# Performance work log

Measured on AMD Instinct MI355X. Metric: run time of the kernel, lower is better.

The kernel has to match this reference:

```python
import jax, jax.numpy as jnp
import numpy as np
import math

B, S, D, H = 4, 2048, 1024, 16
DH = D // H  # 64

def setup_inputs() -> dict:
    key = jax.random.key(0)
    ks = jax.random.split(key, 6)
    return {
        "x": jax.random.normal(ks[0], (B, S, D), dtype=jnp.float32),
        "alibi": jax.random.normal(ks[1], (1, H, S, S), dtype=jnp.float32),
        "w_qkv": jax.random.normal(ks[2], (3 * D, D), dtype=jnp.float32) * 0.02,
        "b_qkv": jax.random.normal(ks[3], (3 * D,), dtype=jnp.float32) * 0.02,
        "w_o": jax.random.normal(ks[4], (D, D), dtype=jnp.float32) * 0.02,
        "b_o": jax.random.normal(ks[5], (D,), dtype=jnp.float32) * 0.02,
    }

def reference(x, alibi, w_qkv, b_qkv, w_o, b_o):
    b, s, d = x.shape
    # torch Linear: y = x @ W.T + b
    qkv = x @ w_qkv.T + b_qkv                       # [B, S, 3D]
    qkv = qkv.reshape(b, s, H, 3, DH)               # interleaved per-head q,k,v
    q = jnp.swapaxes(qkv[:, :, :, 0, :], 1, 2)      # [B, H, S, DH]
    k = jnp.swapaxes(qkv[:, :, :, 1, :], 1, 2)
    v = jnp.swapaxes(qkv[:, :, :, 2, :], 1, 2)
    scores = jnp.einsum("bhqd,bhkd->bhqk", q, k) / math.sqrt(DH)
    attn = jax.nn.softmax(scores + alibi, axis=-1)  # [B, H, S, S]
    o = jnp.einsum("bhqk,bhkd->bhqd", attn, v)      # [B, H, S, DH]
    o = jnp.swapaxes(o, 1, 2).reshape(b, s, d)      # [B, S, D]
    return o @ w_o.T + b_o
```

## Files before the change

kernel.cpp:

```cpp
#include <hip/hip_runtime.h>
#include <stdint.h>

#define S_LEN 2048
#define NH    16
#define NB    4
#define DH    64
#define DMODEL 1024

using bf16x8 = __attribute__((ext_vector_type(8))) __bf16;
using f32x4  = __attribute__((ext_vector_type(4))) float;
using us8    = __attribute__((ext_vector_type(8))) unsigned short;

__device__ __forceinline__ unsigned short f2bf_rne(float f) {
    unsigned u = __builtin_bit_cast(unsigned, f);
    return (unsigned short)((u + 0x7FFFu + ((u >> 16) & 1u)) >> 16);
}

__device__ __forceinline__ bf16x8 ld_bf8(const unsigned short* p) {
    return __builtin_bit_cast(bf16x8, *(const us8*)p);
}

__device__ __forceinline__ f32x4 mfma16(bf16x8 a, bf16x8 b, f32x4 c) {
    return __builtin_amdgcn_mfma_f32_16x16x32_bf16(a, b, c, 0, 0, 0);
}

__device__ __forceinline__ float fast_exp2(float x) {
#if __has_builtin(__builtin_amdgcn_exp2f)
    return __builtin_amdgcn_exp2f(x);
#else
    return __expf(x * 0.69314718056f);
#endif
}

typedef __attribute__((address_space(1))) void* gp1_t;
typedef __attribute__((address_space(3))) void* lp3_t;

__device__ __forceinline__ void gload_lds16(const void* g, void* l) {
    __builtin_amdgcn_global_load_lds((gp1_t)(const_cast<void*>(g)), (lp3_t)l, 16, 0, 0);
}

#define GBAR()  asm volatile("s_barrier" ::: "memory")
#define WAIT6() asm volatile("s_waitcnt vmcnt(6)" ::: "memory")
#define WAIT0() asm volatile("s_waitcnt vmcnt(0)" ::: "memory")

__global__ void cvt_bf16(const float* __restrict__ in, unsigned short* __restrict__ out, int n4) {
    int i = blockIdx.x * 256 + threadIdx.x;
    if (i < n4) {
        float4 v = ((const float4*)in)[i];
        ushort4 o;
        o.x = f2bf_rne(v.x); o.y = f2bf_rne(v.y);
        o.z = f2bf_rne(v.z); o.w = f2bf_rne(v.w);
        ((ushort4*)out)[i] = o;
    }
}

template <int EPI>
__global__ __launch_bounds__(512, 2) void gemm256(
    const unsigned short* __restrict__ A,
    const unsigned short* __restrict__ W,
    const float* __restrict__ bias,
    float* __restrict__ outF,
    unsigned short* __restrict__ Qb,
    unsigned short* __restrict__ Kb,
    unsigned short* __restrict__ Vt,
    int nTilesN)
{
    constexpr int BM = 256, BN = 128, BK = 64;
    constexpr int MI = 4, NJ = 4;
    constexpr int AI = (BM * BK / 8) / 512;
    constexpr int BI = (BN * BK / 8) / 512;

    __shared__ __align__(16) unsigned short As[2][BM * BK];
    __shared__ __align__(16) unsigned short Bs[2][BN * BK];

    const int nwg = gridDim.x;
    const int swz = (blockIdx.x & 7) * (nwg >> 3) + (blockIdx.x >> 3);
    const int bm = swz / nTilesN;
    const int bn = swz % nTilesN;
    const int tileM = bm * BM, tileN = bn * BN;

    const int tid = threadIdx.x, lane = tid & 63, w = tid >> 6;
    const int m16 = lane & 15, quad = lane >> 4;
    const int wm = w >> 1, wn = w & 1;

    f32x4 acc[MI][NJ] = {};

    size_t aoff[AI], boff[BI];
#pragma unroll
    for (int i = 0; i < AI; i++) {
        const int u = (i * 8 + w) * 64 + lane;
        const int row = u >> 3, slot = u & 7;
        aoff[i] = (size_t)(tileM + row) * 1024 + (size_t)((slot ^ (row & 7)) * 8);
    }
#pragma unroll
    for (int i = 0; i < BI; i++) {
        const int u = (i * 8 + w) * 64 + lane;
        const int row = u >> 3, slot = u & 7;
        boff[i] = (size_t)(tileN + row) * 1024 + (size_t)((slot ^ (row & 7)) * 8);
    }

#define STAGE(buf, kk) do {                                               \
        _Pragma("unroll")                                                 \
        for (int i = 0; i < AI; i++)                                      \
            gload_lds16(A + aoff[i] + (kk), &As[buf][(i * 8 + w) * 512]); \
        _Pragma("unroll")                                                 \
        for (int i = 0; i < BI; i++)                                      \
            gload_lds16(W + boff[i] + (kk), &Bs[buf][(i * 8 + w) * 512]); \
    } while (0)

#define COMPUTE(buf) do {                                                          \
        _Pragma("unroll")                                                          \
        for (int ks = 0; ks < 2; ks++) {                                           \
            bf16x8 af[MI], bfv[NJ];                                                \
            _Pragma("unroll")                                                      \
            for (int i = 0; i < MI; i++) {                                         \
                const int R = wm * 64 + i * 16 + m16;                              \
                af[i] = ld_bf8(&As[buf][(R * 8 + ((ks * 4 + quad) ^ (R & 7))) * 8]); \
            }                                                                      \
            _Pragma("unroll")                                                      \
            for (int j = 0; j < NJ; j++) {                                         \
                const int Rb = wn * 64 + j * 16 + m16;                             \
                bfv[j] = ld_bf8(&Bs[buf][(Rb * 8 + ((ks * 4 + quad) ^ (Rb & 7))) * 8]); \
            }                                                                      \
            _Pragma("unroll")                                                      \
            for (int i = 0; i < MI; i++)                                           \
                _Pragma("unroll")                                                  \
                for (int j = 0; j < NJ; j++)                                       \
                    acc[i][j] = mfma16(af[i], bfv[j], acc[i][j]);                  \
        }                                                                          \
    } while (0)

    STAGE(0, 0);
    STAGE(1, 64);
    WAIT6();
    GBAR();

    for (int kk = 0; kk < 1024; kk += 128) {
        COMPUTE(0);
        GBAR();
        if (kk + 128 < 1024) { STAGE(0, kk + 128); WAIT6(); }
        else                 { WAIT0(); }
        GBAR();
        COMPUTE(1);
        if (kk + 128 < 1024) {
            GBAR();
            if (kk + 192 < 1024) { STAGE(1, kk + 192); WAIT6(); }
            else                 { WAIT0(); }
            GBAR();
        }
    }
#undef STAGE
#undef COMPUTE

#pragma unroll
    for (int i = 0; i < MI; i++) {
        const int mrow = tileM + wm * 64 + i * 16 + quad * 4;
#pragma unroll
        for (int j = 0; j < NJ; j++) {
            const int nb0 = tileN + wn * 64 + j * 16;
            const int n = nb0 + m16;
            const float bv = bias[n];
            if (EPI == 0) {
                const int hh = nb0 / 192, rem = nb0 % 192;
                const int t = rem / 64, dbase = rem % 64;
                const int d = dbase + m16;
#pragma unroll
                for (int r = 0; r < 4; r++) {
                    float val = acc[i][j][r] + bv;
                    const int m = mrow + r;
                    const int b_ = m >> 11, s_ = m & 2047;
                    const size_t bh = (size_t)b_ * NH + hh;
                    if (t == 0)
                        Qb[(bh * S_LEN + s_) * DH + d] = f2bf_rne(val * 0.18033688f);
                    else if (t == 1)
                        Kb[(bh * S_LEN + s_) * DH + d] = f2bf_rne(val);
                    else
                        Vt[(bh * DH + d) * S_LEN + s_] = f2bf_rne(val);
                }
            } else {
#pragma unroll
                for (int r = 0; r < 4; r++) {
                    const int m = mrow + r;
                    outF[(size_t)m * DMODEL + n] = acc[i][j][r] + bv;
                }
            }
        }
    }
}

__global__ __launch_bounds__(256, 4) void attn(const unsigned short* __restrict__ Qb,
                                               const unsigned short* __restrict__ Kb,
                                               const unsigned short* __restrict__ Vt,
                                               const float* __restrict__ alibi,
                                               unsigned short* __restrict__ ob) {
    const int blk = blockIdx.x;
    const int xcd = blk & 7;
    const int b_  = (blk >> 3) & 3;
    const int hq  = xcd * 32 + (blk >> 5);
    const int hh  = hq >> 4, qt = hq & 15;
    const int tid = threadIdx.x, lane = tid & 63, w = tid >> 6;
    const int m16 = lane & 15, quad = lane >> 4;
    const int q0 = qt * 128;
    const size_t bh = (size_t)b_ * NH + hh;

    const unsigned short* Qp = Qb + (bh * S_LEN) * DH;
    const unsigned short* Kp = Kb + bh * S_LEN * DH;
    const unsigned short* Vp = Vt + bh * DH * S_LEN;

    __shared__ __align__(16) unsigned short Ks[128 * 64];
    __shared__ __align__(16) unsigned short Vs[64 * 128];
    __shared__ __align__(16) unsigned int   Pl[4][16 * 20];

    bf16x8 qfrag[2][2];
#pragma unroll
    for (int qf = 0; qf < 2; qf++) {
        const unsigned short* qp = Qp + (size_t)(q0 + w * 32 + qf * 16 + m16) * DH + quad * 8;
        qfrag[qf][0] = ld_bf8(qp);
        qfrag[qf][1] = ld_bf8(qp + 32);
    }
    const float* Apq[2];
#pragma unroll
    for (int qf = 0; qf < 2; qf++)
        Apq[qf] = alibi + ((size_t)hh * S_LEN + q0 + w * 32 + qf * 16 + m16) * S_LEN + quad * 4;

    int offk[4], offv[4];
#pragma unroll
    for (int t = 0; t < 4; t++) {
        const int ck = (w * 4 + t) * 64 + lane;
        const int rk = ck >> 3;
        offk[t] = rk * DH + ((ck & 7) ^ (rk & 7)) * 8;
        const int cv = ck;
        const int dv = cv >> 4;
        offv[t] = dv * S_LEN + ((cv & 15) ^ (dv & 15)) * 8;
    }

    const bf16x8 onesf = __builtin_bit_cast(bf16x8, (us8)(0x3F80u));
    f32x4 oacc[2][4] = {};
    f32x4 ssum[2] = {};
    unsigned int* plw = &Pl[w][0];
    const int sA = m16 & 7;

    float4 alc0 = *(const float4*)(Apq[0]);
    float4 alc1 = *(const float4*)(Apq[0] + 16);

    for (int kc = 0; kc < S_LEN; kc += 128) {
        __syncthreads();
#pragma unroll
        for (int t = 0; t < 4; t++)
            gload_lds16(Kp + (size_t)kc * DH + offk[t], &Ks[(w * 4 + t) * 512]);
#pragma unroll
        for (int t = 0; t < 4; t++)
            gload_lds16(Vp + kc + offv[t], &Vs[(w * 4 + t) * 512]);
        __syncthreads();

#pragma unroll
        for (int qf = 0; qf < 2; qf++) {
            const bf16x8 qa = qfrag[qf][0], qb2 = qfrag[qf][1];
#pragma unroll
            for (int kc2 = 0; kc2 < 4; kc2++) {
                const float* nptr = (kc2 < 3) ? (Apq[qf] + kc + (kc2 + 1) * 32)
                                  : (qf == 0) ? (Apq[1] + kc)
                                              : (Apq[0] + ((kc + 128) & (S_LEN - 1)));
                const float4 aln0 = *(const float4*)(nptr);
                const float4 aln1 = *(const float4*)(nptr + 16);

                f32x4 sc[2];
                __builtin_amdgcn_s_setprio(1);
#pragma unroll
                for (int t = 0; t < 2; t++) {
                    const int krow = (kc2 * 2 + t) * 16 + m16;
                    f32x4 z = {};
                    z = mfma16(ld_bf8(&Ks[krow * DH + (quad ^ sA) * 8]), qa, z);
                    z = mfma16(ld_bf8(&Ks[krow * DH + ((quad + 4) ^ sA) * 8]), qb2, z);
                    sc[t] = z;
                }
                __builtin_amdgcn_s_setprio(0);
#pragma unroll
                for (int t = 0; t < 2; t++) {
                    const float4 av = (t == 0) ? alc0 : alc1;
                    float p0 = fast_exp2(__builtin_fmaf(av.x, 1.44269504f, sc[t][0]));
                    float p1 = fast_exp2(__builtin_fmaf(av.y, 1.44269504f, sc[t][1]));
                    float p2 = fast_exp2(__builtin_fmaf(av.z, 1.44269504f, sc[t][2]));
                    float p3 = fast_exp2(__builtin_fmaf(av.w, 1.44269504f, sc[t][3]));
                    uint2 pk;
                    pk.x = (__builtin_bit_cast(unsigned, p0) >> 16) |
                           (__builtin_bit_cast(unsigned, p1) & 0xFFFF0000u);
                    pk.y = (__builtin_bit_cast(unsigned, p2) >> 16) |
                           (__builtin_bit_cast(unsigned, p3) & 0xFFFF0000u);
                    *(uint2*)&plw[m16 * 20 + t * 8 + quad * 2] = pk;
                }
                const bf16x8 pf = ld_bf8((const unsigned short*)&plw[m16 * 20 + quad * 4]);
                __builtin_amdgcn_s_setprio(1);
                ssum[qf] = mfma16(pf, onesf, ssum[qf]);
#pragma unroll
                for (int db = 0; db < 4; db++) {
                    const int vrow = db * 16 + m16;
                    const bf16x8 vf = ld_bf8(&Vs[vrow * 128 + ((kc2 * 4 + quad) ^ m16) * 8]);
                    oacc[qf][db] = mfma16(pf, vf, oacc[qf][db]);
                }
                __builtin_amdgcn_s_setprio(0);

                alc0 = aln0;
                alc1 = aln1;
            }
        }
    }

#pragma unroll
    for (int qf = 0; qf < 2; qf++) {
        f32x4 rinv;
#pragma unroll
        for (int r = 0; r < 4; r++) rinv[r] = 1.0f / ssum[qf][r];
#pragma unroll
        for (int db = 0; db < 4; db++)
#pragma unroll
            for (int r = 0; r < 4; r++) {
                const int q = q0 + w * 32 + qf * 16 + quad * 4 + r;
                ob[((size_t)b_ * S_LEN + q) * DMODEL + hh * DH + db * 16 + m16] =
                    f2bf_rne(oacc[qf][db][r] * rinv[r]);
            }
    }
}

extern "C" void kernel_launch(void* const* d_in, const int* in_sizes, int n_in,
                              void* d_out, int out_size, void* d_ws, size_t ws_size,
                              hipStream_t stream) {
    (void)in_sizes; (void)n_in; (void)out_size; (void)ws_size;
    const float* x      = (const float*)d_in[0];
    const float* alibi  = (const float*)d_in[1];
    const float* w_qkv  = (const float*)d_in[2];
    const float* b_qkv  = (const float*)d_in[3];
    const float* w_o    = (const float*)d_in[4];
    const float* b_o    = (const float*)d_in[5];
    float* out = (float*)d_out;

    char* ws = (char*)d_ws;
    unsigned short* xb    = (unsigned short*)(ws);
    unsigned short* wqkvb = (unsigned short*)(ws + 16777216);
    unsigned short* wob   = (unsigned short*)(ws + 23068672);
    unsigned short* Qb    = (unsigned short*)(ws + 25165824);
    unsigned short* Kb    = (unsigned short*)(ws + 41943040);
    unsigned short* Vt    = (unsigned short*)(ws + 58720256);
    unsigned short* ob    = (unsigned short*)(ws + 75497472);

    cvt_bf16<<<8192, 256, 0, stream>>>(x, xb, 8388608 / 4);
    cvt_bf16<<<3072, 256, 0, stream>>>(w_qkv, wqkvb, 3145728 / 4);
    cvt_bf16<<<1024, 256, 0, stream>>>(w_o, wob, 1048576 / 4);

    gemm256<0><<<768, 512, 0, stream>>>(xb, wqkvb, b_qkv, nullptr, Qb, Kb, Vt, 24);
    attn<<<1024, 256, 0, stream>>>(Qb, Kb, Vt, alibi, ob);
    gemm256<1><<<256, 512, 0, stream>>>(ob, wob, b_o, out, nullptr, nullptr, nullptr, 8);
}
```

Before: 606.6 us.

## Software-pipeline attention P·V MFMAs behind next-step softmax; merge bf16 conversions

The attention inner loop over (qf, kc2) is flattened into eight steps. Each step now issues the P·V and row-sum MFMAs for the previous step's P tile while the QK MFMAs and exp2 for the current tile run, and an epilogue drains the last tile. This aims to hide the dependency chain exp → LDS write → LDS read → MFMA inside a wave, at the cost of keeping one more bf16x8 fragment live. The three fp32→bf16 conversion launches are also merged into one kernel that writes into the contiguous workspace, saving two launches.

```diff
diff --git a/kernel.cpp b/kernel.cpp
--- a/kernel.cpp
+++ b/kernel.cpp
@@ -43,15 +43,19 @@
 #define WAIT6() asm volatile("s_waitcnt vmcnt(6)" ::: "memory")
 #define WAIT0() asm volatile("s_waitcnt vmcnt(0)" ::: "memory")
 
-__global__ void cvt_bf16(const float* __restrict__ in, unsigned short* __restrict__ out, int n4) {
-    int i = blockIdx.x * 256 + threadIdx.x;
-    if (i < n4) {
-        float4 v = ((const float4*)in)[i];
-        ushort4 o;
-        o.x = f2bf_rne(v.x); o.y = f2bf_rne(v.y);
-        o.z = f2bf_rne(v.z); o.w = f2bf_rne(v.w);
-        ((ushort4*)out)[i] = o;
-    }
+__global__ void cvt_all(const float* __restrict__ x, const float* __restrict__ wq,
+                        const float* __restrict__ wo, unsigned short* __restrict__ out) {
+    const int i = blockIdx.x * 256 + threadIdx.x;
+    const float4* src;
+    int o;
+    if (i < 2097152)      { src = (const float4*)x;  o = i; }
+    else if (i < 2883584) { src = (const float4*)wq; o = i - 2097152; }
+    else                  { src = (const float4*)wo; o = i - 2883584; }
+    float4 v = src[o];
+    ushort4 r;
+    r.x = f2bf_rne(v.x); r.y = f2bf_rne(v.y);
+    r.z = f2bf_rne(v.z); r.w = f2bf_rne(v.w);
+    ((ushort4*)out)[i] = r;
 }
 
 template <int EPI>
@@ -254,55 +258,68 @@
         __syncthreads();
 
 #pragma unroll
-        for (int qf = 0; qf < 2; qf++) {
+        for (int s = 0; s < 8; s++) {
+            const int qf = s >> 2, kc2 = s & 3;
             const bf16x8 qa = qfrag[qf][0], qb2 = qfrag[qf][1];
-#pragma unroll
-            for (int kc2 = 0; kc2 < 4; kc2++) {
-                const float* nptr = (kc2 < 3) ? (Apq[qf] + kc + (kc2 + 1) * 32)
-                                  : (qf == 0) ? (Apq[1] + kc)
-                                              : (Apq[0] + ((kc + 128) & (S_LEN - 1)));
-                const float4 aln0 = *(const float4*)(nptr);
-                const float4 aln1 = *(const float4*)(nptr + 16);
-
-                f32x4 sc[2];
+            const float* nptr = (kc2 < 3) ? (Apq[qf] + kc + (kc2 + 1) * 32)
+                              : (qf == 0) ? (Apq[1] + kc)
+                                          : (Apq[0] + ((kc + 128) & (S_LEN - 1)));
+            const float4 aln0 = *(const float4*)(nptr);
+            const float4 aln1 = *(const float4*)(nptr + 16);
+
+            bf16x8 pfp = {};
+            if (s > 0)
+                pfp = ld_bf8((const unsigned short*)&plw[m16 * 20 + quad * 4]);
+
+            f32x4 sc[2];
+            __builtin_amdgcn_s_setprio(1);
+#pragma unroll
+            for (int t = 0; t < 2; t++) {
+                const int krow = (kc2 * 2 + t) * 16 + m16;
+                f32x4 z = {};
+                z = mfma16(ld_bf8(&Ks[krow * DH + (quad ^ sA) * 8]), qa, z);
+                z = mfma16(ld_bf8(&Ks[krow * DH + ((quad + 4) ^ sA) * 8]), qb2, z);
+                sc[t] = z;
+            }
+            __builtin_amdgcn_s_setprio(0);
+#pragma unroll
+            for (int t = 0; t < 2; t++) {
+                const float4 av = (t == 0) ? alc0 : alc1;
+                float p0 = fast_exp2(__builtin_fmaf(av.x, 1.44269504f, sc[t][0]));
+                float p1 = fast_exp2(__builtin_fmaf(av.y, 1.44269504f, sc[t][1]));
+                float p2 = fast_exp2(__builtin_fmaf(av.z, 1.44269504f, sc[t][2]));
+                float p3 = fast_exp2(__builtin_fmaf(av.w, 1.44269504f, sc[t][3]));
+                uint2 pk;
+                pk.x = (__builtin_bit_cast(unsigned, p0) >> 16) |
+                       (__builtin_bit_cast(unsigned, p1) & 0xFFFF0000u);
+                pk.y = (__builtin_bit_cast(unsigned, p2) >> 16) |
+                       (__builtin_bit_cast(unsigned, p3) & 0xFFFF0000u);
+                *(uint2*)&plw[m16 * 20 + t * 8 + quad * 2] = pk;
+            }
+            if (s > 0) {
+                const int kc2p = (s - 1) & 3, qfp = (s - 1) >> 2;
                 __builtin_amdgcn_s_setprio(1);
-#pragma unroll
-                for (int t = 0; t < 2; t++) {
-                    const int krow = (kc2 * 2 + t) * 16 + m16;
-                    f32x4 z = {};
-                    z = mfma16(ld_bf8(&Ks[krow * DH + (quad ^ sA) * 8]), qa, z);
-                    z = mfma16(ld_bf8(&Ks[krow * DH + ((quad + 4) ^ sA) * 8]), qb2, z);
-                    sc[t] = z;
+                ssum[qfp] = mfma16(pfp, onesf, ssum[qfp]);
+#pragma unroll
+                for (int db = 0; db < 4; db++) {
+                    const bf16x8 vf = ld_bf8(&Vs[(db * 16 + m16) * 128 + ((kc2p * 4 + quad) ^ m16) * 8]);
+                    oacc[qfp][db] = mfma16(pfp, vf, oacc[qfp][db]);
                 }
                 __builtin_amdgcn_s_setprio(0);
-#pragma unroll
-                for (int t = 0; t < 2; t++) {
-                    const float4 av = (t == 0) ? alc0 : alc1;
-                    float p0 = fast_exp2(__builtin_fmaf(av.x, 1.44269504f, sc[t][0]));
-                    float p1 = fast_exp2(__builtin_fmaf(av.y, 1.44269504f, sc[t][1]));
-                    float p2 = fast_exp2(__builtin_fmaf(av.z, 1.44269504f, sc[t][2]));
-                    float p3 = fast_exp2(__builtin_fmaf(av.w, 1.44269504f, sc[t][3]));
-                    uint2 pk;
-                    pk.x = (__builtin_bit_cast(unsigned, p0) >> 16) |
-                           (__builtin_bit_cast(unsigned, p1) & 0xFFFF0000u);
-                    pk.y = (__builtin_bit_cast(unsigned, p2) >> 16) |
-                           (__builtin_bit_cast(unsigned, p3) & 0xFFFF0000u);
-                    *(uint2*)&plw[m16 * 20 + t * 8 + quad * 2] = pk;
-                }
-                const bf16x8 pf = ld_bf8((const unsigned short*)&plw[m16 * 20 + quad * 4]);
-                __builtin_amdgcn_s_setprio(1);
-                ssum[qf] = mfma16(pf, onesf, ssum[qf]);
-#pragma unroll
-                for (int db = 0; db < 4; db++) {
-                    const int vrow = db * 16 + m16;
-                    const bf16x8 vf = ld_bf8(&Vs[vrow * 128 + ((kc2 * 4 + quad) ^ m16) * 8]);
-                    oacc[qf][db] = mfma16(pf, vf, oacc[qf][db]);
-                }
-                __builtin_amdgcn_s_setprio(0);
-
-                alc0 = aln0;
-                alc1 = aln1;
-            }
+            }
+            alc0 = aln0;
+            alc1 = aln1;
+        }
+        {
+            const bf16x8 pfp = ld_bf8((const unsigned short*)&plw[m16 * 20 + quad * 4]);
+            __builtin_amdgcn_s_setprio(1);
+            ssum[1] = mfma16(pfp, onesf, ssum[1]);
+#pragma unroll
+            for (int db = 0; db < 4; db++) {
+                const bf16x8 vf = ld_bf8(&Vs[(db * 16 + m16) * 128 + ((12 + quad) ^ m16) * 8]);
+                oacc[1][db] = mfma16(pfp, vf, oacc[1][db]);
+            }
+            __builtin_amdgcn_s_setprio(0);
         }
     }
 
@@ -343,9 +360,7 @@
     unsigned short* Vt    = (unsigned short*)(ws + 58720256);
     unsigned short* ob    = (unsigned short*)(ws + 75497472);
 
-    cvt_bf16<<<8192, 256, 0, stream>>>(x, xb, 8388608 / 4);
-    cvt_bf16<<<3072, 256, 0, stream>>>(w_qkv, wqkvb, 3145728 / 4);
-    cvt_bf16<<<1024, 256, 0, stream>>>(w_o, wob, 1048576 / 4);
+    cvt_all<<<12288, 256, 0, stream>>>(x, w_qkv, w_o, xb);
 
     gemm256<0><<<768, 512, 0, stream>>>(xb, wqkvb, b_qkv, nullptr, Qb, Kb, Vt, 24);
     attn<<<1024, 256, 0, stream>>>(Qb, Kb, Vt, alibi, ob);
```

After: 616.1 us. Within noise of the previous version (+1.6%).
